# Kernel tuning notes

Hardware: AMD Instinct MI355X
Metric: run time of the kernel (lower is better)

The kernel has to match this reference:

```python
import jax, jax.numpy as jnp
import numpy as np

ENERGY_PERCENT = 0.8


def setup_inputs() -> dict:
    key = jax.random.key(0)
    B, T, C = 32, 4096, 128
    x = jax.random.normal(key, (B, T, C), dtype=jnp.float32)
    return {"x": x}


def reference(x):
    # x: [B, T, C]; FFT along time axis.
    T = x.shape[1]
    xf = jnp.fft.rfft(x, axis=1)                      # [B, F, C] complex
    energies = jnp.abs(xf) ** 2                       # [B, F, C]

    # Sort energies descending along freq axis (per batch, per channel).
    sorted_indices = jnp.argsort(-energies, axis=1)   # [B, F, C] int
    sorted_energies = jnp.take_along_axis(energies, sorted_indices, axis=1)

    total_energy = jnp.sum(energies, axis=1, keepdims=True)        # [B, 1, C]
    cumulative = jnp.cumsum(sorted_energies, axis=1)               # [B, F, C]

    # Smallest k such that cumulative energy exceeds energy_percent of total.
    exceeded = cumulative > total_energy * ENERGY_PERCENT          # [B, F, C] bool
    k = jnp.argmax(exceeded, axis=1) + 1                           # [B, C]

    # rank[b, f, c] = position of frequency f in the descending energy order;
    # this is the inverse permutation of sorted_indices (argsort of a permutation).
    rank = jnp.argsort(sorted_indices, axis=1)                     # [B, F, C]

    is_low_freq = rank < k[:, None, :]                             # [B, F, C]

    # Zero out the high-energy ("low-frequency") components -> residual x_var.
    mask = jnp.where(is_low_freq, 0.0, 1.0).astype(x.dtype)        # [B, F, C]
    x_var = jnp.fft.irfft(xf * mask, n=T, axis=1)                  # [B, T, C]
    x_inv = x - x_var
    return (x_var, x_inv)
```

## Files before the change

kernel.cpp:

```cpp
#include <hip/hip_runtime.h>


#define TLEN 4096
#define N2   2048
#define CCH  128
#define BB   32
#define NSER (BB * CCH)
#define HALF 16777216
#define PI_F 3.14159265358979323846f

#define LP(i) ((i) + ((i) >> 5))

__device__ __forceinline__ void cmul(float& r, float& i, float br, float bi) {
  float tr = r * br - i * bi;
  i = r * bi + i * br;
  r = tr;
}

__device__ __forceinline__ void dft4(float vr[4], float vi[4], float s) {
  float t0r = vr[0] + vr[2], t0i = vi[0] + vi[2];
  float t1r = vr[0] - vr[2], t1i = vi[0] - vi[2];
  float t2r = vr[1] + vr[3], t2i = vi[1] + vi[3];
  float d3r = vr[1] - vr[3], d3i = vi[1] - vi[3];
  float t3r = -s * d3i, t3i = s * d3r;
  vr[0] = t0r + t2r; vi[0] = t0i + t2i;
  vr[1] = t1r + t3r; vi[1] = t1i + t3i;
  vr[2] = t0r - t2r; vi[2] = t0i - t2i;
  vr[3] = t1r - t3r; vi[3] = t1i - t3i;
}

__device__ __forceinline__ void dft8(float vr[8], float vi[8], float s) {
  float er[4]  = {vr[0], vr[2], vr[4], vr[6]};
  float ei[4]  = {vi[0], vi[2], vi[4], vi[6]};
  float odr[4] = {vr[1], vr[3], vr[5], vr[7]};
  float odi[4] = {vi[1], vi[3], vi[5], vi[7]};
  dft4(er, ei, s);
  dft4(odr, odi, s);
  const float c = 0.70710678118654752440f;
  float wr[4] = {1.0f, c, 0.0f, -c};
  float wi[4] = {0.0f, s * c, s, s * c};
  #pragma unroll
  for (int k = 0; k < 4; ++k) {
    float tr = wr[k] * odr[k] - wi[k] * odi[k];
    float ti = wr[k] * odi[k] + wi[k] * odr[k];
    vr[k]     = er[k] + tr; vi[k]     = ei[k] + ti;
    vr[k + 4] = er[k] - tr; vi[k + 4] = ei[k] - ti;
  }
}

__device__ __forceinline__ void stage8_first(float* zr, float* zi, int tid, float s) {
  float vr[8], vi[8];
  #pragma unroll
  for (int r = 0; r < 8; ++r) {
    int idx = LP(tid + (r << 8));
    vr[r] = zr[idx]; vi[r] = zi[idx];
  }
  dft8(vr, vi, s);
  __syncthreads();
  #pragma unroll
  for (int r = 0; r < 8; ++r) {
    int idx = LP((tid << 3) + r);
    zr[idx] = vr[r]; zi[idx] = vi[r];
  }
  __syncthreads();
}

template <int NS>
__device__ __forceinline__ void stage8_tw(float* zr, float* zi, int tid, float s) {
  int j = tid;
  int p = j & (NS - 1);
  float vr[8], vi[8];
  #pragma unroll
  for (int r = 0; r < 8; ++r) {
    int idx = LP(j + (r << 8));
    vr[r] = zr[idx]; vi[r] = zi[idx];
  }
  float ang = s * 6.28318530717958647692f * (float)p / (float)(NS * 8);
  float s1, c1; __sincosf(ang, &s1, &c1);
  float c2 = c1 * c1 - s1 * s1, s2 = 2.0f * c1 * s1;
  float c3 = c2 * c1 - s2 * s1, s3 = c2 * s1 + s2 * c1;
  float c4 = c2 * c2 - s2 * s2, s4 = 2.0f * c2 * s2;
  float c5 = c4 * c1 - s4 * s1, s5 = c4 * s1 + s4 * c1;
  float c6 = c4 * c2 - s4 * s2, s6 = c4 * s2 + s4 * c2;
  float c7 = c4 * c3 - s4 * s3, s7 = c4 * s3 + s4 * c3;
  cmul(vr[1], vi[1], c1, s1);
  cmul(vr[2], vi[2], c2, s2);
  cmul(vr[3], vi[3], c3, s3);
  cmul(vr[4], vi[4], c4, s4);
  cmul(vr[5], vi[5], c5, s5);
  cmul(vr[6], vi[6], c6, s6);
  cmul(vr[7], vi[7], c7, s7);
  dft8(vr, vi, s);
  __syncthreads();
  int idxD = ((j - p) << 3) + p;
  #pragma unroll
  for (int r = 0; r < 8; ++r) {
    int idx = LP(idxD + r * NS);
    zr[idx] = vr[r]; zi[idx] = vi[r];
  }
  __syncthreads();
}

__device__ __forceinline__ void stage4_last(float* zr, float* zi, int tid, float s) {
  #pragma unroll
  for (int half = 0; half < 2; ++half) {
    int j = tid + (half << 8);
    float ang = s * PI_F * (float)j * (1.0f / 1024.0f);
    float s1, c1; __sincosf(ang, &s1, &c1);
    float c2 = c1 * c1 - s1 * s1, s2 = 2.0f * c1 * s1;
    float c3 = c2 * c1 - s2 * s1, s3 = c2 * s1 + s2 * c1;
    float vr[4], vi[4];
    #pragma unroll
    for (int r = 0; r < 4; ++r) {
      int idx = LP(j + (r << 9));
      vr[r] = zr[idx]; vi[r] = zi[idx];
    }
    cmul(vr[1], vi[1], c1, s1);
    cmul(vr[2], vi[2], c2, s2);
    cmul(vr[3], vi[3], c3, s3);
    dft4(vr, vi, s);
    #pragma unroll
    for (int r = 0; r < 4; ++r) {
      int idx = LP(j + (r << 9));
      zr[idx] = vr[r]; zi[idx] = vi[r];
    }
  }
  __syncthreads();
}

__device__ __forceinline__ void fft2048(float* zr, float* zi, int tid, float s) {
  stage8_first(zr, zi, tid, s);
  stage8_tw<8>(zr, zi, tid, s);
  stage8_tw<64>(zr, zi, tid, s);
  stage4_last(zr, zi, tid, s);
}

__device__ __forceinline__ float block_sum(float v, float* red, int tid, int bank) {
  #pragma unroll
  for (int o = 32; o > 0; o >>= 1) v += __shfl_down(v, o, 64);
  if ((tid & 63) == 0) red[(bank << 2) + (tid >> 6)] = v;
  __syncthreads();
  int b4 = bank << 2;
  return red[b4] + red[b4 + 1] + red[b4 + 2] + red[b4 + 3];
}

__global__ __launch_bounds__(256) void fourier_filter_series(float* __restrict__ buf) {
  __shared__ float zr[2113], zi[2113];
  __shared__ float red[8];
  int tid = threadIdx.x;
  float* p = buf + (size_t)blockIdx.x * TLEN;

  const float2* p2 = (const float2*)p;
  #pragma unroll
  for (int k = tid; k < N2; k += 256) {
    float2 v = p2[k];
    zr[LP(k)] = v.x; zi[LP(k)] = v.y;
  }
  __syncthreads();

  fft2048(zr, zi, tid, -1.0f);

  float eb[9];
  eb[8] = 0.0f;
  const float RC  = 0.92387953251128675613f;
  const float RSn = -0.38268343236508977173f;
  float ws, wc;
  __sincosf(-PI_F * (float)tid * (1.0f / 2048.0f), &ws, &wc);
  #pragma unroll
  for (int jj = 0; jj < 4; ++jj) {
    int k = tid + (jj << 8);
    int mkz = (N2 - k) & (N2 - 1);
    int ik = LP(k), im = LP(N2 - k);
    float akr = zr[ik],      aki = zi[ik];
    float bkr = zr[LP(mkz)], bki = zi[LP(mkz)];
    float Er  = 0.5f * (akr + bkr);
    float Ei  = 0.5f * (aki - bki);
    float Or_ = 0.5f * (aki + bki);
    float Oi  = 0.5f * (bkr - akr);
    float tr = wc * Or_ - ws * Oi;
    float ti = wc * Oi + ws * Or_;
    float x0r = Er + tr, x0i = Ei + ti;
    float x1r = Er - tr, x1i = ti - Ei;
    zr[ik] = x0r; zi[ik] = x0i;
    zr[im] = x1r; zi[im] = x1i;
    eb[2 * jj]     = x0r * x0r + x0i * x0i;
    eb[2 * jj + 1] = x1r * x1r + x1i * x1i;
    float nwc = wc * RC - ws * RSn;
    ws = wc * RSn + ws * RC; wc = nwc;
  }
  if (tid == 0) {
    int i4 = LP(1024);
    float re = zr[i4], im_ = zi[i4];
    zi[i4] = -im_;
    eb[8] = re * re + im_ * im_;
  }

  float tloc = 0.0f;
  #pragma unroll
  for (int s = 0; s < 9; ++s) tloc += eb[s];
  float total = block_sum(tloc, red, tid, 0);
  float thresh = 0.8f * total;

  unsigned lo = 0u, hi = 0x7F7FFFFFu;
  for (int it = 0; it < 31; ++it) {
    unsigned mid = (lo + hi + 1u) >> 1;
    float tau = __uint_as_float(mid);
    float loc = 0.0f;
    #pragma unroll
    for (int s = 0; s < 9; ++s) loc += (eb[s] >= tau) ? eb[s] : 0.0f;
    float ssum = block_sum(loc, red, tid, (it + 1) & 1);
    if (ssum > thresh) lo = mid; else hi = mid - 1;
  }
  float tau = __uint_as_float(lo);

  const float RSp = 0.38268343236508977173f;
  __sincosf(PI_F * (float)tid * (1.0f / 2048.0f), &ws, &wc);
  #pragma unroll
  for (int jj = 0; jj < 4; ++jj) {
    int k = tid + (jj << 8);
    int ik = LP(k), im = LP(N2 - k);
    float xkr = zr[ik], xki = zi[ik];
    float xmr = zr[im], xmi = zi[im];
    float ekk = xkr * xkr + xki * xki;
    float emm = xmr * xmr + xmi * xmi;
    if (ekk >= tau) { xkr = 0.0f; xki = 0.0f; }
    if (emm >= tau) { xmr = 0.0f; xmi = 0.0f; }
    float Er = 0.5f * (xkr + xmr);
    float Ei = 0.5f * (xki - xmi);
    float Br = 0.5f * (xkr - xmr);
    float Bi = 0.5f * (xki + xmi);
    float Or_ = wc * Br - ws * Bi;
    float Oi  = wc * Bi + ws * Br;
    zr[ik] = Er - Oi;  zi[ik] = Ei + Or_;
    zr[im] = Er + Oi;  zi[im] = Or_ - Ei;
    float nwc = wc * RC - ws * RSp;
    ws = wc * RSp + ws * RC; wc = nwc;
  }
  if (tid == 0) {
    int i4 = LP(1024);
    float re = zr[i4], im_ = zi[i4];
    float e = re * re + im_ * im_;
    if (e >= tau) { re = 0.0f; im_ = 0.0f; }
    zr[i4] = re; zi[i4] = -im_;
  }
  __syncthreads();

  fft2048(zr, zi, tid, 1.0f);

  const float scale = 1.0f / 2048.0f;
  float2* po = (float2*)p;
  #pragma unroll
  for (int k = tid; k < N2; k += 256) {
    float2 v;
    v.x = zr[LP(k)] * scale;
    v.y = zi[LP(k)] * scale;
    po[k] = v;
  }
}

__global__ __launch_bounds__(256) void transpose_fwd(const float* __restrict__ x, float* __restrict__ xT) {
  __shared__ float tile[64][65];
  int t0 = blockIdx.x << 6, c0 = blockIdx.y << 6, b = blockIdx.z;
  int m = threadIdx.x & 15, q = threadIdx.x >> 4;
  #pragma unroll
  for (int r = 0; r < 4; ++r) {
    int t = q + (r << 4);
    float4 v = *(const float4*)(x + ((size_t)b * TLEN + t0 + t) * CCH + c0 + (m << 2));
    tile[t][(m << 2) + 0] = v.x; tile[t][(m << 2) + 1] = v.y;
    tile[t][(m << 2) + 2] = v.z; tile[t][(m << 2) + 3] = v.w;
  }
  __syncthreads();
  #pragma unroll
  for (int r = 0; r < 4; ++r) {
    int c = q + (r << 4);
    int t4 = m << 2;
    float4 v;
    v.x = tile[t4 + 0][c]; v.y = tile[t4 + 1][c];
    v.z = tile[t4 + 2][c]; v.w = tile[t4 + 3][c];
    *(float4*)(xT + ((size_t)b * CCH + c0 + c) * TLEN + t0 + t4) = v;
  }
}

__global__ __launch_bounds__(256) void finalize_t(const float* __restrict__ xvT, const float* __restrict__ x,
                                                  float* __restrict__ xvar, float* __restrict__ xinv) {
  __shared__ float tile[64][65];
  int t0 = blockIdx.x << 6, c0 = blockIdx.y << 6, b = blockIdx.z;
  int m = threadIdx.x & 15, q = threadIdx.x >> 4;
  #pragma unroll
  for (int r = 0; r < 4; ++r) {
    int c = q + (r << 4);
    int t4 = m << 2;
    float4 v = *(const float4*)(xvT + ((size_t)b * CCH + c0 + c) * TLEN + t0 + t4);
    tile[t4 + 0][c] = v.x; tile[t4 + 1][c] = v.y;
    tile[t4 + 2][c] = v.z; tile[t4 + 3][c] = v.w;
  }
  __syncthreads();
  #pragma unroll
  for (int r = 0; r < 4; ++r) {
    int t = q + (r << 4);
    int c4 = m << 2;
    float4 v;
    v.x = tile[t][c4 + 0]; v.y = tile[t][c4 + 1];
    v.z = tile[t][c4 + 2]; v.w = tile[t][c4 + 3];
    size_t off = ((size_t)b * TLEN + t0 + t) * CCH + c0 + c4;
    float4 xv = *(const float4*)(x + off);
    *(float4*)(xvar + off) = v;
    *(float4*)(xinv + off) = make_float4(xv.x - v.x, xv.y - v.y, xv.z - v.z, xv.w - v.w);
  }
}

__global__ __launch_bounds__(256) void transpose_back(const float* __restrict__ xvT, float* __restrict__ xvar) {
  __shared__ float tile[64][65];
  int t0 = blockIdx.x << 6, c0 = blockIdx.y << 6, b = blockIdx.z;
  int m = threadIdx.x & 15, q = threadIdx.x >> 4;
  #pragma unroll
  for (int r = 0; r < 4; ++r) {
    int c = q + (r << 4);
    int t4 = m << 2;
    float4 v = *(const float4*)(xvT + ((size_t)b * CCH + c0 + c) * TLEN + t0 + t4);
    tile[t4 + 0][c] = v.x; tile[t4 + 1][c] = v.y;
    tile[t4 + 2][c] = v.z; tile[t4 + 3][c] = v.w;
  }
  __syncthreads();
  #pragma unroll
  for (int r = 0; r < 4; ++r) {
    int t = q + (r << 4);
    int c4 = m << 2;
    float4 v;
    v.x = tile[t][c4 + 0]; v.y = tile[t][c4 + 1];
    v.z = tile[t][c4 + 2]; v.w = tile[t][c4 + 3];
    size_t off = ((size_t)b * TLEN + t0 + t) * CCH + c0 + c4;
    *(float4*)(xvar + off) = v;
  }
}

__global__ __launch_bounds__(256) void sub_kernel(const float4* __restrict__ x, const float4* __restrict__ xv,
                                                  float4* __restrict__ xi, int n4) {
  int i = blockIdx.x * 256 + threadIdx.x;
  if (i < n4) {
    float4 a = x[i], b = xv[i];
    xi[i] = make_float4(a.x - b.x, a.y - b.y, a.z - b.z, a.w - b.w);
  }
}

extern "C" void kernel_launch(void* const* d_in, const int* in_sizes, int n_in,
                              void* d_out, int out_size, void* d_ws, size_t ws_size,
                              hipStream_t stream) {
  const float* x = (const float*)d_in[0];
  float* out  = (float*)d_out;
  float* xvar = out;
  float* xinv = out + HALF;

  bool use_ws = ws_size >= (size_t)NSER * TLEN * sizeof(float);
  float* buf = use_ws ? (float*)d_ws : xinv;

  dim3 tgrid(TLEN / 64, CCH / 64, BB);
  transpose_fwd<<<tgrid, 256, 0, stream>>>(x, buf);
  fourier_filter_series<<<NSER, 256, 0, stream>>>(buf);
  if (use_ws) {
    finalize_t<<<tgrid, 256, 0, stream>>>(buf, x, xvar, xinv);
  } else {
    transpose_back<<<tgrid, 256, 0, stream>>>(buf, xvar);
    sub_kernel<<<(HALF / 4 + 255) / 256, 256, 0, stream>>>((const float4*)x, (const float4*)xvar,
                                                           (float4*)xinv, HALF / 4);
  }
}
```

Before: 303.3 us.

## Use time-block slab layout for intermediate buffer to coalesce transposes

Changes the intermediate buffer from a per-series contiguous [B][C][T] layout to [B][time-block][C][64] slabs. Each transpose block now handles a full 64×128 tile covering all channels, with 512 threads. The FFT kernel gathers each series from 256-byte chunks spread across slabs. The aim is to make transpose reads and writes fully contiguous per block and to let the non-workspace fallback share the in-place finalize path. The risk is LDS bank conflicts in the new transpose writes and more scattered global accesses in the FFT load and store.

New measurement: 300.7 us. About the same (-0.8%).

```diff
diff --git a/kernel.cpp b/kernel.cpp
--- a/kernel.cpp
+++ b/kernel.cpp
@@ -8,6 +8,9 @@
 #define NSER (BB * CCH)
 #define HALF 16777216
 #define PI_F 3.14159265358979323846f
+#define NT   64
+#define TS   64
+#define SLAB (CCH * TS)
 
 #define LP(i) ((i) + ((i) >> 5))
 
@@ -148,12 +151,14 @@
   __shared__ float zr[2113], zi[2113];
   __shared__ float red[8];
   int tid = threadIdx.x;
-  float* p = buf + (size_t)blockIdx.x * TLEN;
-
-  const float2* p2 = (const float2*)p;
-  #pragma unroll
-  for (int k = tid; k < N2; k += 256) {
-    float2 v = p2[k];
+  int b = blockIdx.x >> 7, c = blockIdx.x & 127;
+  float* bufp = buf + (size_t)b * (NT * SLAB) + (size_t)c * TS;
+
+  #pragma unroll
+  for (int j = 0; j < 8; ++j) {
+    int k = tid + (j << 8);
+    int off = ((k >> 5) << 13) + ((k & 31) << 1);
+    float2 v = *(const float2*)(bufp + off);
     zr[LP(k)] = v.x; zi[LP(k)] = v.y;
   }
   __syncthreads();
@@ -248,98 +253,72 @@
   fft2048(zr, zi, tid, 1.0f);
 
   const float scale = 1.0f / 2048.0f;
-  float2* po = (float2*)p;
-  #pragma unroll
-  for (int k = tid; k < N2; k += 256) {
+  #pragma unroll
+  for (int j = 0; j < 8; ++j) {
+    int k = tid + (j << 8);
+    int off = ((k >> 5) << 13) + ((k & 31) << 1);
     float2 v;
     v.x = zr[LP(k)] * scale;
     v.y = zi[LP(k)] * scale;
-    po[k] = v;
-  }
-}
-
-__global__ __launch_bounds__(256) void transpose_fwd(const float* __restrict__ x, float* __restrict__ xT) {
-  __shared__ float tile[64][65];
-  int t0 = blockIdx.x << 6, c0 = blockIdx.y << 6, b = blockIdx.z;
-  int m = threadIdx.x & 15, q = threadIdx.x >> 4;
-  #pragma unroll
-  for (int r = 0; r < 4; ++r) {
-    int t = q + (r << 4);
-    float4 v = *(const float4*)(x + ((size_t)b * TLEN + t0 + t) * CCH + c0 + (m << 2));
-    tile[t][(m << 2) + 0] = v.x; tile[t][(m << 2) + 1] = v.y;
-    tile[t][(m << 2) + 2] = v.z; tile[t][(m << 2) + 3] = v.w;
-  }
-  __syncthreads();
-  #pragma unroll
-  for (int r = 0; r < 4; ++r) {
-    int c = q + (r << 4);
-    int t4 = m << 2;
+    *(float2*)(bufp + off) = v;
+  }
+}
+
+__global__ __launch_bounds__(512) void transpose_fwd(const float* __restrict__ x, float* __restrict__ buf) {
+  __shared__ float lds[CCH * 65];
+  int tb = blockIdx.x, b = blockIdx.y;
+  const float* xp = x + ((size_t)b * TLEN + (size_t)tb * TS) * CCH;
+  #pragma unroll
+  for (int it = 0; it < 4; ++it) {
+    int idx = threadIdx.x + (it << 9);
+    int r = idx >> 5, c4 = (idx & 31) << 2;
+    float4 v = *(const float4*)(xp + (size_t)r * CCH + c4);
+    lds[(c4 + 0) * 65 + r] = v.x;
+    lds[(c4 + 1) * 65 + r] = v.y;
+    lds[(c4 + 2) * 65 + r] = v.z;
+    lds[(c4 + 3) * 65 + r] = v.w;
+  }
+  __syncthreads();
+  float* op = buf + ((size_t)b * NT + tb) * SLAB;
+  #pragma unroll
+  for (int it = 0; it < 4; ++it) {
+    int idx = threadIdx.x + (it << 9);
+    int c = idx >> 4, s4 = (idx & 15) << 2;
     float4 v;
-    v.x = tile[t4 + 0][c]; v.y = tile[t4 + 1][c];
-    v.z = tile[t4 + 2][c]; v.w = tile[t4 + 3][c];
-    *(float4*)(xT + ((size_t)b * CCH + c0 + c) * TLEN + t0 + t4) = v;
-  }
-}
-
-__global__ __launch_bounds__(256) void finalize_t(const float* __restrict__ xvT, const float* __restrict__ x,
+    v.x = lds[c * 65 + s4 + 0];
+    v.y = lds[c * 65 + s4 + 1];
+    v.z = lds[c * 65 + s4 + 2];
+    v.w = lds[c * 65 + s4 + 3];
+    *(float4*)(op + c * TS + s4) = v;
+  }
+}
+
+__global__ __launch_bounds__(512) void finalize_t(const float* __restrict__ buf, const float* __restrict__ x,
                                                   float* __restrict__ xvar, float* __restrict__ xinv) {
-  __shared__ float tile[64][65];
-  int t0 = blockIdx.x << 6, c0 = blockIdx.y << 6, b = blockIdx.z;
-  int m = threadIdx.x & 15, q = threadIdx.x >> 4;
-  #pragma unroll
-  for (int r = 0; r < 4; ++r) {
-    int c = q + (r << 4);
-    int t4 = m << 2;
-    float4 v = *(const float4*)(xvT + ((size_t)b * CCH + c0 + c) * TLEN + t0 + t4);
-    tile[t4 + 0][c] = v.x; tile[t4 + 1][c] = v.y;
-    tile[t4 + 2][c] = v.z; tile[t4 + 3][c] = v.w;
-  }
-  __syncthreads();
-  #pragma unroll
-  for (int r = 0; r < 4; ++r) {
-    int t = q + (r << 4);
-    int c4 = m << 2;
-    float4 v;
-    v.x = tile[t][c4 + 0]; v.y = tile[t][c4 + 1];
-    v.z = tile[t][c4 + 2]; v.w = tile[t][c4 + 3];
-    size_t off = ((size_t)b * TLEN + t0 + t) * CCH + c0 + c4;
+  __shared__ float lds[TS * 132];
+  int tb = blockIdx.x, b = blockIdx.y;
+  const float* ip = buf + ((size_t)b * NT + tb) * SLAB;
+  #pragma unroll
+  for (int it = 0; it < 4; ++it) {
+    int idx = threadIdx.x + (it << 9);
+    int c = idx >> 4, s4 = (idx & 15) << 2;
+    float4 v = *(const float4*)(ip + c * TS + s4);
+    lds[(s4 + 0) * 132 + c] = v.x;
+    lds[(s4 + 1) * 132 + c] = v.y;
+    lds[(s4 + 2) * 132 + c] = v.z;
+    lds[(s4 + 3) * 132 + c] = v.w;
+  }
+  __syncthreads();
+  size_t rowbase = ((size_t)b * TLEN + (size_t)tb * TS) * CCH;
+  #pragma unroll
+  for (int it = 0; it < 4; ++it) {
+    int idx = threadIdx.x + (it << 9);
+    int t = idx >> 5, c4 = (idx & 31) << 2;
+    float4 v = *(const float4*)(&lds[t * 132 + c4]);
+    size_t off = rowbase + (size_t)t * CCH + c4;
     float4 xv = *(const float4*)(x + off);
     *(float4*)(xvar + off) = v;
     *(float4*)(xinv + off) = make_float4(xv.x - v.x, xv.y - v.y, xv.z - v.z, xv.w - v.w);
-  }
-}
-
-__global__ __launch_bounds__(256) void transpose_back(const float* __restrict__ xvT, float* __restrict__ xvar) {
-  __shared__ float tile[64][65];
-  int t0 = blockIdx.x << 6, c0 = blockIdx.y << 6, b = blockIdx.z;
-  int m = threadIdx.x & 15, q = threadIdx.x >> 4;
-  #pragma unroll
-  for (int r = 0; r < 4; ++r) {
-    int c = q + (r << 4);
-    int t4 = m << 2;
-    float4 v = *(const float4*)(xvT + ((size_t)b * CCH + c0 + c) * TLEN + t0 + t4);
-    tile[t4 + 0][c] = v.x; tile[t4 + 1][c] = v.y;
-    tile[t4 + 2][c] = v.z; tile[t4 + 3][c] = v.w;
-  }
-  __syncthreads();
-  #pragma unroll
-  for (int r = 0; r < 4; ++r) {
-    int t = q + (r << 4);
-    int c4 = m << 2;
-    float4 v;
-    v.x = tile[t][c4 + 0]; v.y = tile[t][c4 + 1];
-    v.z = tile[t][c4 + 2]; v.w = tile[t][c4 + 3];
-    size_t off = ((size_t)b * TLEN + t0 + t) * CCH + c0 + c4;
-    *(float4*)(xvar + off) = v;
-  }
-}
-
-__global__ __launch_bounds__(256) void sub_kernel(const float4* __restrict__ x, const float4* __restrict__ xv,
-                                                  float4* __restrict__ xi, int n4) {
-  int i = blockIdx.x * 256 + threadIdx.x;
-  if (i < n4) {
-    float4 a = x[i], b = xv[i];
-    xi[i] = make_float4(a.x - b.x, a.y - b.y, a.z - b.z, a.w - b.w);
   }
 }
 
@@ -351,17 +330,11 @@
   float* xvar = out;
   float* xinv = out + HALF;
 
-  bool use_ws = ws_size >= (size_t)NSER * TLEN * sizeof(float);
+  bool use_ws = ws_size >= (size_t)HALF * sizeof(float);
   float* buf = use_ws ? (float*)d_ws : xinv;
 
-  dim3 tgrid(TLEN / 64, CCH / 64, BB);
-  transpose_fwd<<<tgrid, 256, 0, stream>>>(x, buf);
+  dim3 tgrid(NT, BB);
+  transpose_fwd<<<tgrid, 512, 0, stream>>>(x, buf);
   fourier_filter_series<<<NSER, 256, 0, stream>>>(buf);
-  if (use_ws) {
-    finalize_t<<<tgrid, 256, 0, stream>>>(buf, x, xvar, xinv);
-  } else {
-    transpose_back<<<tgrid, 256, 0, stream>>>(buf, xvar);
-    sub_kernel<<<(HALF / 4 + 255) / 256, 256, 0, stream>>>((const float4*)x, (const float4*)xvar,
-                                                           (float4*)xinv, HALF / 4);
-  }
-}
+  finalize_t<<<tgrid, 512, 0, stream>>>(buf, x, xvar, xinv);
+}
```
